# Performance work log

Hardware: AMD Instinct MI355X
Metric: run time of the kernel (lower is better)

The kernel has to match this reference:

```python
import jax, jax.numpy as jnp
import numpy as np

NUM_HEADS = 32
NUM_KV_HEADS = 8
HEAD_DIM = 128
SEQ = 2048
MAX_SLOTS = 4096
SCALE = float(1.0 / np.sqrt(HEAD_DIM))  # attn_scale
G = NUM_HEADS // NUM_KV_HEADS  # num_queries_per_kv


def setup_inputs() -> dict:
    key = jax.random.key(0)
    k1, k2, k3 = jax.random.split(key, 3)
    q = jax.random.normal(k1, (SEQ, NUM_HEADS, HEAD_DIM), dtype=jnp.float32)
    k = jax.random.normal(k2, (SEQ, NUM_KV_HEADS, HEAD_DIM), dtype=jnp.float32)
    v = jax.random.normal(k3, (SEQ, NUM_KV_HEADS, HEAD_DIM), dtype=jnp.float32)
    k_cache = jnp.zeros((MAX_SLOTS, NUM_KV_HEADS, HEAD_DIM), dtype=jnp.float32)
    v_cache = jnp.zeros((MAX_SLOTS, NUM_KV_HEADS, HEAD_DIM), dtype=jnp.float32)
    slot_mapping = jnp.arange(SEQ, dtype=jnp.int64)  # contiguous block_table slots
    return {"q": q, "k": k, "v": v, "k_cache": k_cache, "v_cache": v_cache,
            "slot_mapping": slot_mapping}


def reference(q, k, v, k_cache, v_cache, slot_mapping):
    # prefill: scatter-write new K/V into the paged cache (self.k_cache[slot_mapping] = k)
    kc = k_cache.at[slot_mapping].set(k)
    vc = v_cache.at[slot_mapping].set(v)
    # gather K/V back from the cache via slot mapping (paged gather pattern)
    k_attn = kc[slot_mapping]  # (S, Hkv, D) == k since slots are unique
    v_attn = vc[slot_mapping]
    # GQA: repeat_interleave kv heads to match query heads
    kr = jnp.repeat(k_attn, G, axis=1)  # (S, H, D)
    vr = jnp.repeat(v_attn, G, axis=1)
    # scores: (H, Sq, Sk), naive full materialization as in the original
    scores = jnp.einsum('qhd,khd->hqk', q, kr) * SCALE
    sq, sk = q.shape[0], k_attn.shape[0]
    mask = jnp.tril(jnp.ones((sq, sk), dtype=bool))  # causal (num_query_tokens > 1)
    scores = jnp.where(mask[None, :, :], scores, -jnp.inf)
    weights = jax.nn.softmax(scores, axis=-1)
    out = jnp.einsum('hqk,khd->qhd', weights, vr)  # (S, H, D)
    return out
```

## Files before the change

kernel.cpp:

```cpp
#include <hip/hip_runtime.h>
#include <hip/hip_bf16.h>

#define SEQ 2048
#define QSTR 4096
#define CSCALE 0.1275174364688796f

typedef __attribute__((ext_vector_type(8)))  short short8;
typedef __attribute__((ext_vector_type(4)))  float f32x4;
typedef __attribute__((ext_vector_type(16))) float f32x16;

union PF8 { unsigned u[4]; short8 s; };

__device__ __forceinline__ unsigned short f2bf(float f) {
    union { __hip_bfloat16 b; unsigned short u; } cv;
    cv.b = __float2bfloat16(f);
    return cv.u;
}
__device__ __forceinline__ float bf2f(unsigned short u) {
    unsigned v = ((unsigned)u) << 16;
    return __builtin_bit_cast(float, v);
}

__device__ __forceinline__ void gload16(const unsigned short* g, unsigned short* l) {
    __builtin_amdgcn_global_load_lds(
        (const __attribute__((address_space(1))) void*)g,
        (__attribute__((address_space(3))) void*)l, 16, 0, 0);
}

__global__ void prep_k(const float* __restrict__ Kg, unsigned short* __restrict__ Kb) {
    int gi = blockIdx.x * 256 + threadIdx.x;
    int kv = gi >> 8;
    int rem = gi & 255;
    int hk = rem >> 5;
    int d4 = rem & 31;
    f32x4 k4 = *(const f32x4*)(Kg + ((size_t)kv * 8 + hk) * 128 + 4 * d4);
    ushort4 u = make_ushort4(f2bf(k4[0]), f2bf(k4[1]), f2bf(k4[2]), f2bf(k4[3]));
    *(ushort4*)(Kb + ((size_t)hk * SEQ + kv) * 128 + 4 * d4) = u;
}

__global__ void prep_v(const float* __restrict__ Vg, unsigned short* __restrict__ Vtb) {
    const int hk  = blockIdx.x >> 5;
    const int kvb = blockIdx.x & 31;
    __shared__ unsigned short T[128][72];
    const int t = threadIdx.x;
    #pragma unroll
    for (int i = 0; i < 8; ++i) {
        int idx = t + 256 * i;
        int r = idx >> 5, d4 = idx & 31;
        f32x4 v = *(const f32x4*)(Vg + ((size_t)(kvb * 64 + r) * 8 + hk) * 128 + 4 * d4);
        T[4 * d4 + 0][r] = f2bf(v[0]);
        T[4 * d4 + 1][r] = f2bf(v[1]);
        T[4 * d4 + 2][r] = f2bf(v[2]);
        T[4 * d4 + 3][r] = f2bf(v[3]);
    }
    __syncthreads();
    #pragma unroll
    for (int i = 0; i < 8; ++i) {
        int idx = t + 256 * i;
        int d = idx >> 4, c4 = idx & 15;
        ushort4 u = *(ushort4*)&T[d][4 * c4];
        *(ushort4*)(Vtb + ((size_t)hk * 128 + d) * SEQ + kvb * 64 + 4 * c4) = u;
    }
}

__launch_bounds__(256, 2)
__global__ void attn_fwd(const float* __restrict__ Qg,
                         const unsigned short* __restrict__ Kb,
                         const unsigned short* __restrict__ Vtb,
                         float* __restrict__ Og) {
    const int bid = blockIdx.x;
    const int p   = bid >> 5;
    const int h   = bid & 31;
    const int hk  = h >> 2;
    const int qbB = 31 - p;
    const int qbA = p;
    const int nsB = 32 - p;

    const int tid  = threadIdx.x;
    const int w    = tid >> 6;
    const int b    = w & 1;
    const int hf   = w >> 1;
    const int lane = tid & 63;
    const int q5   = lane & 31;
    const int t5   = lane >> 5;

    __shared__ unsigned short Ks[2][64][128];
    __shared__ unsigned short Vp[2][64][128];
    __shared__ float mstat[2][4][32];
    __shared__ unsigned short Otb[32][136];

    short8 qf[8];
    auto LOADQ = [&](int qb) __attribute__((always_inline)) {
        const float* qp = Qg + (size_t)(qb * 64 + 32 * b + q5) * QSTR + h * 128 + 8 * t5;
        #pragma unroll
        for (int st = 0; st < 8; ++st) {
            f32x4 a = *(const f32x4*)(qp + 16 * st);
            f32x4 c = *(const f32x4*)(qp + 16 * st + 4);
            short8 f;
            f[0] = (short)f2bf(a[0] * CSCALE); f[1] = (short)f2bf(a[1] * CSCALE);
            f[2] = (short)f2bf(a[2] * CSCALE); f[3] = (short)f2bf(a[3] * CSCALE);
            f[4] = (short)f2bf(c[0] * CSCALE); f[5] = (short)f2bf(c[1] * CSCALE);
            f[6] = (short)f2bf(c[2] * CSCALE); f[7] = (short)f2bf(c[3] * CSCALE);
            qf[st] = f;
        }
    };

    auto ISSUE = [&](int kv0, int bb) __attribute__((always_inline)) {
        #pragma unroll
        for (int p4 = 0; p4 < 4; ++p4) {
            int row = 16 * w + 4 * p4 + (lane >> 4);
            const unsigned short* g = Kb +
                ((size_t)hk * SEQ + kv0 + row) * 128 + 8 * ((lane & 15) ^ (row & 15));
            gload16(g, &Ks[bb][16 * w + 4 * p4][0]);
        }
        #pragma unroll
        for (int p4 = 0; p4 < 4; ++p4) {
            int r  = 16 * w + 4 * p4 + (lane >> 4);
            int gg = lane & 15;
            int d  = 2 * r + (gg >> 3);
            int c  = (gg & 7) ^ (r & 7);
            const unsigned short* g = Vtb +
                ((size_t)hk * 128 + d) * SEQ + kv0 + 8 * c;
            gload16(g, &Vp[bb][16 * w + 4 * p4][0]);
        }
    };

    f32x16 oacc[4];
    float m, l;
    auto RESET = [&]() __attribute__((always_inline)) {
        #pragma unroll
        for (int dt = 0; dt < 4; ++dt)
            #pragma unroll
            for (int r = 0; r < 16; ++r) oacc[dt][r] = 0.f;
        m = -1e30f; l = 0.f;
    };

    auto EPI = [&](int qb) __attribute__((always_inline)) {
        if (t5 == 0) mstat[0][w][q5] = m;
        asm volatile("s_waitcnt lgkmcnt(0)" ::: "memory");
        __builtin_amdgcn_sched_barrier(0);
        __builtin_amdgcn_s_barrier();
        const float mo = mstat[0][w ^ 2][q5];
        const float M  = fmaxf(m, mo);
        const float sc = exp2f(m - M);
        #pragma unroll
        for (int dt = 0; dt < 4; ++dt)
            #pragma unroll
            for (int r = 0; r < 16; ++r) oacc[dt][r] *= sc;
        const float lp = l * sc;
        if (t5 == 0) mstat[1][w][q5] = lp;
        asm volatile("s_waitcnt lgkmcnt(0)" ::: "memory");
        __builtin_amdgcn_sched_barrier(0);
        __builtin_amdgcn_s_barrier();
        const float rl = 1.0f / (lp + mstat[1][w ^ 2][q5]);

        #pragma unroll 1
        for (int bb = 0; bb < 2; ++bb) {
            if (w == 2 + bb) {
                #pragma unroll
                for (int dt = 0; dt < 4; ++dt)
                    #pragma unroll
                    for (int ii = 0; ii < 4; ++ii) {
                        ushort4 u = make_ushort4(
                            f2bf(oacc[dt][4 * ii + 0]), f2bf(oacc[dt][4 * ii + 1]),
                            f2bf(oacc[dt][4 * ii + 2]), f2bf(oacc[dt][4 * ii + 3]));
                        *(ushort4*)&Otb[q5][32 * dt + 8 * ii + 4 * t5] = u;
                    }
            }
            asm volatile("s_waitcnt lgkmcnt(0)" ::: "memory");
            __builtin_amdgcn_sched_barrier(0);
            __builtin_amdgcn_s_barrier();
            if (w == bb) {
                #pragma unroll
                for (int dt = 0; dt < 4; ++dt)
                    #pragma unroll
                    for (int ii = 0; ii < 4; ++ii) {
                        ushort4 o1 = *(ushort4*)&Otb[q5][32 * dt + 8 * ii + 4 * t5];
                        ushort4 u = make_ushort4(
                            f2bf((oacc[dt][4 * ii + 0] + bf2f(o1.x)) * rl),
                            f2bf((oacc[dt][4 * ii + 1] + bf2f(o1.y)) * rl),
                            f2bf((oacc[dt][4 * ii + 2] + bf2f(o1.z)) * rl),
                            f2bf((oacc[dt][4 * ii + 3] + bf2f(o1.w)) * rl));
                        *(ushort4*)&Otb[q5][32 * dt + 8 * ii + 4 * t5] = u;
                    }
            }
            asm volatile("s_waitcnt lgkmcnt(0)" ::: "memory");
            __builtin_amdgcn_sched_barrier(0);
            __builtin_amdgcn_s_barrier();
            {
                const int r  = tid >> 3;
                const int c0 = 16 * (tid & 7);
                float* og = Og + (size_t)(qb * 64 + 32 * bb + r) * QSTR + h * 128 + c0;
                #pragma unroll
                for (int j = 0; j < 4; ++j) {
                    ushort4 u = *(ushort4*)&Otb[r][c0 + 4 * j];
                    f32x4 v;
                    v[0] = bf2f(u.x); v[1] = bf2f(u.y);
                    v[2] = bf2f(u.z); v[3] = bf2f(u.w);
                    *(f32x4*)(og + 4 * j) = v;
                }
            }
            asm volatile("s_waitcnt lgkmcnt(0)" ::: "memory");
            __builtin_amdgcn_sched_barrier(0);
            __builtin_amdgcn_s_barrier();
        }
    };

    LOADQ(qbB);
    #pragma unroll
    for (int st = 0; st < 8; ++st) asm volatile("" :: "v"(qf[st]));
    asm volatile("s_waitcnt vmcnt(0)" ::: "memory");
    RESET();

    ISSUE(0, 0);
    ISSUE(64, 1);

    for (int s = 0; s < 33; ++s) {
        if (s == nsB) {
            LOADQ(qbA);
            EPI(qbB);
            RESET();
        }
        const bool isB = (s < nsB);
        const int kv0  = isB ? 64 * s : 64 * (s - nsB);
        const int qb   = isB ? qbB : qbA;
        const int q0w  = qb * 64 + 32 * b;
        const int buf  = s & 1;

        if (s + 1 < 33) asm volatile("s_waitcnt vmcnt(8)" ::: "memory");
        else            asm volatile("s_waitcnt vmcnt(0)" ::: "memory");
        __builtin_amdgcn_s_barrier();

        const int kvh = kv0 + 32 * hf;
        if (kvh <= q0w + 31) {
            f32x16 sac;
            #pragma unroll
            for (int r = 0; r < 16; ++r) sac[r] = 0.f;
            __builtin_amdgcn_s_setprio(1);
            #pragma unroll
            for (int st = 0; st < 8; ++st) {
                short8 kf = *(const short8*)
                    &Ks[buf][32 * hf + q5][8 * ((2 * st + t5) ^ (q5 & 15))];
                sac = __builtin_amdgcn_mfma_f32_32x32x16_bf16(kf, qf[st], sac, 0, 0, 0);
            }
            __builtin_amdgcn_s_setprio(0);

            if (kvh + 31 > q0w) {
                const int qrow = q0w + q5;
                #pragma unroll
                for (int r = 0; r < 16; ++r) {
                    int kv = kvh + (r & 3) + 8 * (r >> 2) + 4 * t5;
                    if (kv > qrow) sac[r] = -1e30f;
                }
            }

            float m8[8], m4[4], m2[2];
            #pragma unroll
            for (int i = 0; i < 8; ++i) m8[i] = fmaxf(sac[i], sac[i + 8]);
            #pragma unroll
            for (int i = 0; i < 4; ++i) m4[i] = fmaxf(m8[i], m8[i + 4]);
            m2[0] = fmaxf(m4[0], m4[2]); m2[1] = fmaxf(m4[1], m4[3]);
            float mx = fmaxf(m2[0], m2[1]);
            mx = fmaxf(mx, __shfl_xor(mx, 32));

            const bool skip = __all(mx <= m + 11.0f);
            float fac = 1.0f;
            if (!skip) {
                float mn = fmaxf(m, mx);
                fac = exp2f(m - mn);
                m = mn;
            }

            #pragma unroll
            for (int r = 0; r < 16; ++r) sac[r] = exp2f(sac[r] - m);
            float s8[8], s4[4], s2[2];
            #pragma unroll
            for (int i = 0; i < 8; ++i) s8[i] = sac[i] + sac[i + 8];
            #pragma unroll
            for (int i = 0; i < 4; ++i) s4[i] = s8[i] + s8[i + 4];
            s2[0] = s4[0] + s4[2]; s2[1] = s4[1] + s4[3];
            float ps = s2[0] + s2[1];
            ps += __shfl_xor(ps, 32);
            if (!skip) {
                l = l * fac + ps;
                #pragma unroll
                for (int dt = 0; dt < 4; ++dt)
                    #pragma unroll
                    for (int r = 0; r < 16; ++r) oacc[dt][r] *= fac;
            } else {
                l += ps;
            }

            unsigned pkw[8];
            #pragma unroll
            for (int rp = 0; rp < 8; ++rp)
                pkw[rp] = (unsigned)f2bf(sac[2 * rp]) |
                          ((unsigned)f2bf(sac[2 * rp + 1]) << 16);

            unsigned xp[8];
            #pragma unroll
            for (int i = 0; i < 8; ++i)
                xp[i] = (unsigned)__shfl_xor((int)pkw[i], 32);

            PF8 pf[2];
            #pragma unroll
            for (int ks = 0; ks < 2; ++ks) {
                #pragma unroll
                for (int j = 0; j < 4; ++j) {
                    const int ib = (j & 1) + 4 * ks;
                    const unsigned own_lo = pkw[ib];
                    const unsigned own_hi = pkw[ib + 2];
                    const unsigned par_lo = xp[ib];
                    const unsigned par_hi = xp[ib + 2];
                    pf[ks].u[j] = (j < 2) ? (t5 ? par_hi : own_lo)
                                          : (t5 ? own_hi : par_lo);
                }
            }

            __builtin_amdgcn_s_setprio(1);
            #pragma unroll
            for (int dt = 0; dt < 4; ++dt) {
                #pragma unroll
                for (int ks = 0; ks < 2; ++ks) {
                    const int gg = 8 * (q5 & 1) +
                        ((4 * hf + 2 * ks + t5) ^ ((q5 >> 1) & 7));
                    short8 vf = *(const short8*)
                        &Vp[buf][16 * dt + (q5 >> 1)][8 * gg];
                    oacc[dt] = __builtin_amdgcn_mfma_f32_32x32x16_bf16(vf, pf[ks].s, oacc[dt], 0, 0, 0);
                }
            }
            __builtin_amdgcn_s_setprio(0);
        }

        asm volatile("" ::: "memory");
        __builtin_amdgcn_s_barrier();
        if (s + 2 < 33) {
            const int s2 = s + 2;
            ISSUE((s2 < nsB) ? 64 * s2 : 64 * (s2 - nsB), s & 1);
        }
    }

    EPI(qbA);
}

extern "C" void kernel_launch(void* const* d_in, const int* in_sizes, int n_in,
                              void* d_out, int out_size, void* d_ws, size_t ws_size,
                              hipStream_t stream) {
    const float* q = (const float*)d_in[0];
    const float* k = (const float*)d_in[1];
    const float* v = (const float*)d_in[2];
    float* out = (float*)d_out;
    unsigned short* Kb  = (unsigned short*)d_ws;
    unsigned short* Vtb = Kb + (size_t)8 * SEQ * 128;
    prep_k<<<dim3(2048), 256, 0, stream>>>(k, Kb);
    prep_v<<<dim3(256), 256, 0, stream>>>(v, Vtb);
    attn_fwd<<<dim3(512), 256, 0, stream>>>(q, Kb, Vtb, out);
}
```

Baseline: 90.90 us.

## Load K/V fragments directly into registers, drop LDS staging, use 32-row query tiles

Removes the shared-memory double-buffered K/V staging with async global-to-LDS loads. Each wave now reads its K and transposed-V MFMA operands straight from global memory into registers and prefetches the next tiles in software. Query tiles shrink to 32 rows, with 2-wave blocks of 128 threads and 1024 blocks, pairing tiles p and 63-p for causal balance. This drops LDS traffic and per-iteration barriers, but K/V reuse across waves now depends on the L2/L1 caches and register pressure rises.

```diff
diff --git a/kernel.cpp b/kernel.cpp
--- a/kernel.cpp
+++ b/kernel.cpp
@@ -19,12 +19,6 @@
 __device__ __forceinline__ float bf2f(unsigned short u) {
     unsigned v = ((unsigned)u) << 16;
     return __builtin_bit_cast(float, v);
-}
-
-__device__ __forceinline__ void gload16(const unsigned short* g, unsigned short* l) {
-    __builtin_amdgcn_global_load_lds(
-        (const __attribute__((address_space(1))) void*)g,
-        (__attribute__((address_space(3))) void*)l, 16, 0, 0);
 }
 
 __global__ void prep_k(const float* __restrict__ Kg, unsigned short* __restrict__ Kb) {
@@ -63,7 +57,7 @@
     }
 }
 
-__launch_bounds__(256, 2)
+__launch_bounds__(128, 2)
 __global__ void attn_fwd(const float* __restrict__ Qg,
                          const unsigned short* __restrict__ Kb,
                          const unsigned short* __restrict__ Vtb,
@@ -72,75 +66,179 @@
     const int p   = bid >> 5;
     const int h   = bid & 31;
     const int hk  = h >> 2;
-    const int qbB = 31 - p;
-    const int qbA = p;
-    const int nsB = 32 - p;
+    const int tb  = 63 - p;
+    const int ta  = p;
 
     const int tid  = threadIdx.x;
-    const int w    = tid >> 6;
-    const int b    = w & 1;
-    const int hf   = w >> 1;
+    const int wk   = tid >> 6;
     const int lane = tid & 63;
     const int q5   = lane & 31;
     const int t5   = lane >> 5;
 
-    __shared__ unsigned short Ks[2][64][128];
-    __shared__ unsigned short Vp[2][64][128];
-    __shared__ float mstat[2][4][32];
+    __shared__ float mstat[2][2][32];
     __shared__ unsigned short Otb[32][136];
 
-    short8 qf[8];
-    auto LOADQ = [&](int qb) __attribute__((always_inline)) {
-        const float* qp = Qg + (size_t)(qb * 64 + 32 * b + q5) * QSTR + h * 128 + 8 * t5;
-        #pragma unroll
-        for (int st = 0; st < 8; ++st) {
-            f32x4 a = *(const f32x4*)(qp + 16 * st);
-            f32x4 c = *(const f32x4*)(qp + 16 * st + 4);
-            short8 f;
-            f[0] = (short)f2bf(a[0] * CSCALE); f[1] = (short)f2bf(a[1] * CSCALE);
-            f[2] = (short)f2bf(a[2] * CSCALE); f[3] = (short)f2bf(a[3] * CSCALE);
-            f[4] = (short)f2bf(c[0] * CSCALE); f[5] = (short)f2bf(c[1] * CSCALE);
-            f[6] = (short)f2bf(c[2] * CSCALE); f[7] = (short)f2bf(c[3] * CSCALE);
-            qf[st] = f;
-        }
-    };
-
-    auto ISSUE = [&](int kv0, int bb) __attribute__((always_inline)) {
-        #pragma unroll
-        for (int p4 = 0; p4 < 4; ++p4) {
-            int row = 16 * w + 4 * p4 + (lane >> 4);
-            const unsigned short* g = Kb +
-                ((size_t)hk * SEQ + kv0 + row) * 128 + 8 * ((lane & 15) ^ (row & 15));
-            gload16(g, &Ks[bb][16 * w + 4 * p4][0]);
-        }
-        #pragma unroll
-        for (int p4 = 0; p4 < 4; ++p4) {
-            int r  = 16 * w + 4 * p4 + (lane >> 4);
-            int gg = lane & 15;
-            int d  = 2 * r + (gg >> 3);
-            int c  = (gg & 7) ^ (r & 7);
-            const unsigned short* g = Vtb +
-                ((size_t)hk * 128 + d) * SEQ + kv0 + 8 * c;
-            gload16(g, &Vp[bb][16 * w + 4 * p4][0]);
-        }
-    };
-
+    const unsigned short* Kh = Kb  + (size_t)hk * SEQ * 128;
+    const unsigned short* Vh = Vtb + (size_t)hk * 128 * SEQ;
+
+    short8 kA[8], kB[8], vR[8], qf[8];
     f32x16 oacc[4];
     float m, l;
-    auto RESET = [&]() __attribute__((always_inline)) {
+
+    auto LOADK = [&](short8 (&ks8)[8], int kv0) __attribute__((always_inline)) {
+        const unsigned short* kp = Kh + (size_t)(kv0 + q5) * 128 + 8 * t5;
+        #pragma unroll
+        for (int st = 0; st < 8; ++st)
+            ks8[st] = *(const short8*)(kp + 16 * st);
+    };
+    auto LOADV = [&](int kv0) __attribute__((always_inline)) {
+        #pragma unroll
+        for (int dt = 0; dt < 4; ++dt)
+            #pragma unroll
+            for (int ks = 0; ks < 2; ++ks)
+                vR[2 * dt + ks] = *(const short8*)
+                    (Vh + (size_t)(32 * dt + q5) * SEQ + kv0 + 16 * ks + 8 * t5);
+    };
+
+    auto STEP = [&](short8 (&kset)[8], int j, int q0, int qt, int nw)
+        __attribute__((always_inline)) {
+        const int kv0 = 32 * (2 * j + wk);
+
+        f32x16 sac;
+        #pragma unroll
+        for (int r = 0; r < 16; ++r) sac[r] = 0.f;
+        __builtin_amdgcn_s_setprio(1);
+        #pragma unroll
+        for (int st = 0; st < 8; ++st)
+            sac = __builtin_amdgcn_mfma_f32_32x32x16_bf16(kset[st], qf[st], sac, 0, 0, 0);
+        __builtin_amdgcn_s_setprio(0);
+
+        if (j + 2 < nw) LOADK(kset, 32 * (2 * j + 4 + wk));
+
+        if (kv0 + 31 > q0) {
+            const int qrow = q0 + q5;
+            #pragma unroll
+            for (int r = 0; r < 16; ++r) {
+                int kv = kv0 + (r & 3) + 8 * (r >> 2) + 4 * t5;
+                if (kv > qrow) sac[r] = -1e30f;
+            }
+        }
+
+        float m8[8], m4[4], m2[2];
+        #pragma unroll
+        for (int i = 0; i < 8; ++i) m8[i] = fmaxf(sac[i], sac[i + 8]);
+        #pragma unroll
+        for (int i = 0; i < 4; ++i) m4[i] = fmaxf(m8[i], m8[i + 4]);
+        m2[0] = fmaxf(m4[0], m4[2]); m2[1] = fmaxf(m4[1], m4[3]);
+        float mx = fmaxf(m2[0], m2[1]);
+        mx = fmaxf(mx, __shfl_xor(mx, 32));
+
+        const bool skip = __all(mx <= m + 11.0f);
+        float fac = 1.0f;
+        if (!skip) {
+            float mn = fmaxf(m, mx);
+            fac = exp2f(m - mn);
+            m = mn;
+        }
+
+        #pragma unroll
+        for (int r = 0; r < 16; ++r) sac[r] = exp2f(sac[r] - m);
+        float s8[8], s4[4], s2[2];
+        #pragma unroll
+        for (int i = 0; i < 8; ++i) s8[i] = sac[i] + sac[i + 8];
+        #pragma unroll
+        for (int i = 0; i < 4; ++i) s4[i] = s8[i] + s8[i + 4];
+        s2[0] = s4[0] + s4[2]; s2[1] = s4[1] + s4[3];
+        float ps = s2[0] + s2[1];
+        ps += __shfl_xor(ps, 32);
+        if (!skip) {
+            l = l * fac + ps;
+            #pragma unroll
+            for (int dt = 0; dt < 4; ++dt)
+                #pragma unroll
+                for (int r = 0; r < 16; ++r) oacc[dt][r] *= fac;
+        } else {
+            l += ps;
+        }
+
+        unsigned pkw[8];
+        #pragma unroll
+        for (int rp = 0; rp < 8; ++rp)
+            pkw[rp] = (unsigned)f2bf(sac[2 * rp]) |
+                      ((unsigned)f2bf(sac[2 * rp + 1]) << 16);
+
+        unsigned xp[8];
+        #pragma unroll
+        for (int i = 0; i < 8; ++i)
+            xp[i] = (unsigned)__shfl_xor((int)pkw[i], 32);
+
+        PF8 pf[2];
+        #pragma unroll
+        for (int ks = 0; ks < 2; ++ks) {
+            #pragma unroll
+            for (int j4 = 0; j4 < 4; ++j4) {
+                const int ib = (j4 & 1) + 4 * ks;
+                const unsigned own_lo = pkw[ib];
+                const unsigned own_hi = pkw[ib + 2];
+                const unsigned par_lo = xp[ib];
+                const unsigned par_hi = xp[ib + 2];
+                pf[ks].u[j4] = (j4 < 2) ? (t5 ? par_hi : own_lo)
+                                        : (t5 ? own_hi : par_lo);
+            }
+        }
+
+        __builtin_amdgcn_s_setprio(1);
+        #pragma unroll
+        for (int dt = 0; dt < 4; ++dt)
+            #pragma unroll
+            for (int ks = 0; ks < 2; ++ks)
+                oacc[dt] = __builtin_amdgcn_mfma_f32_32x32x16_bf16(
+                    vR[2 * dt + ks], pf[ks].s, oacc[dt], 0, 0, 0);
+        __builtin_amdgcn_s_setprio(0);
+
+        if (j + 1 < nw) LOADV(32 * (2 * j + 2 + wk));
+    };
+
+    #pragma unroll 1
+    for (int ph = 0; ph < 2; ++ph) {
+        const int qt = ph ? ta : tb;
+        const int q0 = 32 * qt;
+        const int nw = (qt + 2 - wk) >> 1;
+
+        {
+            const float* qp = Qg + (size_t)(q0 + q5) * QSTR + h * 128 + 8 * t5;
+            #pragma unroll
+            for (int st = 0; st < 8; ++st) {
+                f32x4 a = *(const f32x4*)(qp + 16 * st);
+                f32x4 c = *(const f32x4*)(qp + 16 * st + 4);
+                short8 f;
+                f[0] = (short)f2bf(a[0] * CSCALE); f[1] = (short)f2bf(a[1] * CSCALE);
+                f[2] = (short)f2bf(a[2] * CSCALE); f[3] = (short)f2bf(a[3] * CSCALE);
+                f[4] = (short)f2bf(c[0] * CSCALE); f[5] = (short)f2bf(c[1] * CSCALE);
+                f[6] = (short)f2bf(c[2] * CSCALE); f[7] = (short)f2bf(c[3] * CSCALE);
+                qf[st] = f;
+            }
+        }
         #pragma unroll
         for (int dt = 0; dt < 4; ++dt)
             #pragma unroll
             for (int r = 0; r < 16; ++r) oacc[dt][r] = 0.f;
         m = -1e30f; l = 0.f;
-    };
-
-    auto EPI = [&](int qb) __attribute__((always_inline)) {
-        if (t5 == 0) mstat[0][w][q5] = m;
-        asm volatile("s_waitcnt lgkmcnt(0)" ::: "memory");
-        __builtin_amdgcn_sched_barrier(0);
-        __builtin_amdgcn_s_barrier();
-        const float mo = mstat[0][w ^ 2][q5];
+
+        if (nw > 0) {
+            LOADK(kA, 32 * wk);
+            LOADV(32 * wk);
+            if (nw > 1) LOADK(kB, 32 * (2 + wk));
+            #pragma unroll 1
+            for (int j = 0; j < nw; j += 2) {
+                STEP(kA, j, q0, qt, nw);
+                if (j + 1 < nw) STEP(kB, j + 1, q0, qt, nw);
+            }
+        }
+
+        if (t5 == 0) mstat[0][wk][q5] = m;
+        __syncthreads();
+        const float mo = mstat[0][wk ^ 1][q5];
         const float M  = fmaxf(m, mo);
         const float sc = exp2f(m - M);
         #pragma unroll
@@ -148,199 +246,52 @@
             #pragma unroll
             for (int r = 0; r < 16; ++r) oacc[dt][r] *= sc;
         const float lp = l * sc;
-        if (t5 == 0) mstat[1][w][q5] = lp;
-        asm volatile("s_waitcnt lgkmcnt(0)" ::: "memory");
-        __builtin_amdgcn_sched_barrier(0);
-        __builtin_amdgcn_s_barrier();
-        const float rl = 1.0f / (lp + mstat[1][w ^ 2][q5]);
-
-        #pragma unroll 1
-        for (int bb = 0; bb < 2; ++bb) {
-            if (w == 2 + bb) {
+        if (t5 == 0) mstat[1][wk][q5] = lp;
+        __syncthreads();
+        const float rl = 1.0f / (lp + mstat[1][wk ^ 1][q5]);
+
+        if (wk == 1) {
+            #pragma unroll
+            for (int dt = 0; dt < 4; ++dt)
                 #pragma unroll
-                for (int dt = 0; dt < 4; ++dt)
-                    #pragma unroll
-                    for (int ii = 0; ii < 4; ++ii) {
-                        ushort4 u = make_ushort4(
-                            f2bf(oacc[dt][4 * ii + 0]), f2bf(oacc[dt][4 * ii + 1]),
-                            f2bf(oacc[dt][4 * ii + 2]), f2bf(oacc[dt][4 * ii + 3]));
-                        *(ushort4*)&Otb[q5][32 * dt + 8 * ii + 4 * t5] = u;
-                    }
-            }
-            asm volatile("s_waitcnt lgkmcnt(0)" ::: "memory");
-            __builtin_amdgcn_sched_barrier(0);
-            __builtin_amdgcn_s_barrier();
-            if (w == bb) {
+                for (int ii = 0; ii < 4; ++ii) {
+                    ushort4 u = make_ushort4(
+                        f2bf(oacc[dt][4 * ii + 0]), f2bf(oacc[dt][4 * ii + 1]),
+                        f2bf(oacc[dt][4 * ii + 2]), f2bf(oacc[dt][4 * ii + 3]));
+                    *(ushort4*)&Otb[q5][32 * dt + 8 * ii + 4 * t5] = u;
+                }
+        }
+        __syncthreads();
+        if (wk == 0) {
+            #pragma unroll
+            for (int dt = 0; dt < 4; ++dt)
                 #pragma unroll
-                for (int dt = 0; dt < 4; ++dt)
-                    #pragma unroll
-                    for (int ii = 0; ii < 4; ++ii) {
-                        ushort4 o1 = *(ushort4*)&Otb[q5][32 * dt + 8 * ii + 4 * t5];
-                        ushort4 u = make_ushort4(
-                            f2bf((oacc[dt][4 * ii + 0] + bf2f(o1.x)) * rl),
-                            f2bf((oacc[dt][4 * ii + 1] + bf2f(o1.y)) * rl),
-                            f2bf((oacc[dt][4 * ii + 2] + bf2f(o1.z)) * rl),
-                            f2bf((oacc[dt][4 * ii + 3] + bf2f(o1.w)) * rl));
-                        *(ushort4*)&Otb[q5][32 * dt + 8 * ii + 4 * t5] = u;
-                    }
-            }
-            asm volatile("s_waitcnt lgkmcnt(0)" ::: "memory");
-            __builtin_amdgcn_sched_barrier(0);
-            __builtin_amdgcn_s_barrier();
-            {
-                const int r  = tid >> 3;
-                const int c0 = 16 * (tid & 7);
-                float* og = Og + (size_t)(qb * 64 + 32 * bb + r) * QSTR + h * 128 + c0;
-                #pragma unroll
-                for (int j = 0; j < 4; ++j) {
-                    ushort4 u = *(ushort4*)&Otb[r][c0 + 4 * j];
-                    f32x4 v;
-                    v[0] = bf2f(u.x); v[1] = bf2f(u.y);
-                    v[2] = bf2f(u.z); v[3] = bf2f(u.w);
-                    *(f32x4*)(og + 4 * j) = v;
+                for (int ii = 0; ii < 4; ++ii) {
+                    ushort4 o1 = *(ushort4*)&Otb[q5][32 * dt + 8 * ii + 4 * t5];
+                    ushort4 u = make_ushort4(
+                        f2bf((oacc[dt][4 * ii + 0] + bf2f(o1.x)) * rl),
+                        f2bf((oacc[dt][4 * ii + 1] + bf2f(o1.y)) * rl),
+                        f2bf((oacc[dt][4 * ii + 2] + bf2f(o1.z)) * rl),
+                        f2bf((oacc[dt][4 * ii + 3] + bf2f(o1.w)) * rl));
+                    *(ushort4*)&Otb[q5][32 * dt + 8 * ii + 4 * t5] = u;
                 }
-            }
-            asm volatile("s_waitcnt lgkmcnt(0)" ::: "memory");
-            __builtin_amdgcn_sched_barrier(0);
-            __builtin_amdgcn_s_barrier();
-        }
-    };
-
-    LOADQ(qbB);
-    #pragma unroll
-    for (int st = 0; st < 8; ++st) asm volatile("" :: "v"(qf[st]));
-    asm volatile("s_waitcnt vmcnt(0)" ::: "memory");
-    RESET();
-
-    ISSUE(0, 0);
-    ISSUE(64, 1);
-
-    for (int s = 0; s < 33; ++s) {
-        if (s == nsB) {
-            LOADQ(qbA);
-            EPI(qbB);
-            RESET();
-        }
-        const bool isB = (s < nsB);
-        const int kv0  = isB ? 64 * s : 64 * (s - nsB);
-        const int qb   = isB ? qbB : qbA;
-        const int q0w  = qb * 64 + 32 * b;
-        const int buf  = s & 1;
-
-        if (s + 1 < 33) asm volatile("s_waitcnt vmcnt(8)" ::: "memory");
-        else            asm volatile("s_waitcnt vmcnt(0)" ::: "memory");
-        __builtin_amdgcn_s_barrier();
-
-        const int kvh = kv0 + 32 * hf;
-        if (kvh <= q0w + 31) {
-            f32x16 sac;
-            #pragma unroll
-            for (int r = 0; r < 16; ++r) sac[r] = 0.f;
-            __builtin_amdgcn_s_setprio(1);
-            #pragma unroll
-            for (int st = 0; st < 8; ++st) {
-                short8 kf = *(const short8*)
-                    &Ks[buf][32 * hf + q5][8 * ((2 * st + t5) ^ (q5 & 15))];
-                sac = __builtin_amdgcn_mfma_f32_32x32x16_bf16(kf, qf[st], sac, 0, 0, 0);
-            }
-            __builtin_amdgcn_s_setprio(0);
-
-            if (kvh + 31 > q0w) {
-                const int qrow = q0w + q5;
-                #pragma unroll
-                for (int r = 0; r < 16; ++r) {
-                    int kv = kvh + (r & 3) + 8 * (r >> 2) + 4 * t5;
-                    if (kv > qrow) sac[r] = -1e30f;
-                }
-            }
-
-            float m8[8], m4[4], m2[2];
-            #pragma unroll
-            for (int i = 0; i < 8; ++i) m8[i] = fmaxf(sac[i], sac[i + 8]);
-            #pragma unroll
-            for (int i = 0; i < 4; ++i) m4[i] = fmaxf(m8[i], m8[i + 4]);
-            m2[0] = fmaxf(m4[0], m4[2]); m2[1] = fmaxf(m4[1], m4[3]);
-            float mx = fmaxf(m2[0], m2[1]);
-            mx = fmaxf(mx, __shfl_xor(mx, 32));
-
-            const bool skip = __all(mx <= m + 11.0f);
-            float fac = 1.0f;
-            if (!skip) {
-                float mn = fmaxf(m, mx);
-                fac = exp2f(m - mn);
-                m = mn;
-            }
-
-            #pragma unroll
-            for (int r = 0; r < 16; ++r) sac[r] = exp2f(sac[r] - m);
-            float s8[8], s4[4], s2[2];
-            #pragma unroll
-            for (int i = 0; i < 8; ++i) s8[i] = sac[i] + sac[i + 8];
-            #pragma unroll
-            for (int i = 0; i < 4; ++i) s4[i] = s8[i] + s8[i + 4];
-            s2[0] = s4[0] + s4[2]; s2[1] = s4[1] + s4[3];
-            float ps = s2[0] + s2[1];
-            ps += __shfl_xor(ps, 32);
-            if (!skip) {
-                l = l * fac + ps;
-                #pragma unroll
-                for (int dt = 0; dt < 4; ++dt)
-                    #pragma unroll
-                    for (int r = 0; r < 16; ++r) oacc[dt][r] *= fac;
-            } else {
-                l += ps;
-            }
-
-            unsigned pkw[8];
-            #pragma unroll
-            for (int rp = 0; rp < 8; ++rp)
-                pkw[rp] = (unsigned)f2bf(sac[2 * rp]) |
-                          ((unsigned)f2bf(sac[2 * rp + 1]) << 16);
-
-            unsigned xp[8];
-            #pragma unroll
-            for (int i = 0; i < 8; ++i)
-                xp[i] = (unsigned)__shfl_xor((int)pkw[i], 32);
-
-            PF8 pf[2];
-            #pragma unroll
-            for (int ks = 0; ks < 2; ++ks) {
-                #pragma unroll
-                for (int j = 0; j < 4; ++j) {
-                    const int ib = (j & 1) + 4 * ks;
-                    const unsigned own_lo = pkw[ib];
-                    const unsigned own_hi = pkw[ib + 2];
-                    const unsigned par_lo = xp[ib];
-                    const unsigned par_hi = xp[ib + 2];
-                    pf[ks].u[j] = (j < 2) ? (t5 ? par_hi : own_lo)
-                                          : (t5 ? own_hi : par_lo);
-                }
-            }
-
-            __builtin_amdgcn_s_setprio(1);
-            #pragma unroll
-            for (int dt = 0; dt < 4; ++dt) {
-                #pragma unroll
-                for (int ks = 0; ks < 2; ++ks) {
-                    const int gg = 8 * (q5 & 1) +
-                        ((4 * hf + 2 * ks + t5) ^ ((q5 >> 1) & 7));
-                    short8 vf = *(const short8*)
-                        &Vp[buf][16 * dt + (q5 >> 1)][8 * gg];
-                    oacc[dt] = __builtin_amdgcn_mfma_f32_32x32x16_bf16(vf, pf[ks].s, oacc[dt], 0, 0, 0);
-                }
-            }
-            __builtin_amdgcn_s_setprio(0);
-        }
-
-        asm volatile("" ::: "memory");
-        __builtin_amdgcn_s_barrier();
-        if (s + 2 < 33) {
-            const int s2 = s + 2;
-            ISSUE((s2 < nsB) ? 64 * s2 : 64 * (s2 - nsB), s & 1);
-        }
+        }
+        __syncthreads();
+        {
+            #pragma unroll
+            for (int i = 0; i < 8; ++i) {
+                int ck = tid + 128 * i;
+                int r  = ck >> 5;
+                int c4 = (ck & 31) * 4;
+                ushort4 u = *(ushort4*)&Otb[r][c4];
+                f32x4 v;
+                v[0] = bf2f(u.x); v[1] = bf2f(u.y);
+                v[2] = bf2f(u.z); v[3] = bf2f(u.w);
+                *(f32x4*)(Og + (size_t)(q0 + r) * QSTR + h * 128 + c4) = v;
+            }
+        }
+        __syncthreads();
     }
-
-    EPI(qbA);
 }
 
 extern "C" void kernel_launch(void* const* d_in, const int* in_sizes, int n_in,
@@ -354,5 +305,5 @@
     unsigned short* Vtb = Kb + (size_t)8 * SEQ * 128;
     prep_k<<<dim3(2048), 256, 0, stream>>>(k, Kb);
     prep_v<<<dim3(256), 256, 0, stream>>>(v, Vtb);
-    attn_fwd<<<dim3(512), 256, 0, stream>>>(q, Kb, Vtb, out);
-}
+    attn_fwd<<<dim3(1024), 128, 0, stream>>>(q, Kb, Vtb, out);
+}
```

Result: slower. 155.8 us (+71.4%).

## Prefetch next tile's K/V MFMA fragments from LDS into registers

Applied to the files above, without the earlier changes.

Each iteration's K and V MFMA operands are now read from shared memory into register arrays at the end of the previous iteration, right after a single barrier. That barrier also publishes the next tile, and the global-to-LDS load for the tile after it is then issued. This cuts the loop from two barriers to one and moves the LDS fragment reads off the critical path ahead of the QK and PV MFMAs. In exchange it adds about 64 VGPRs of live fragment state, which risks lower occupancy or spills. It also waits for all outstanding vector memory before each barrier instead of keeping one tile in flight.

```diff
diff --git a/kernel.cpp b/kernel.cpp
--- a/kernel.cpp
+++ b/kernel.cpp
@@ -89,7 +89,8 @@
     __shared__ float mstat[2][4][32];
     __shared__ unsigned short Otb[32][136];
 
-    short8 qf[8];
+    short8 qf[8], kreg[8], vreg[8];
+
     auto LOADQ = [&](int qb) __attribute__((always_inline)) {
         const float* qp = Qg + (size_t)(qb * 64 + 32 * b + q5) * QSTR + h * 128 + 8 * t5;
         #pragma unroll
@@ -123,6 +124,22 @@
                 ((size_t)hk * 128 + d) * SEQ + kv0 + 8 * c;
             gload16(g, &Vp[bb][16 * w + 4 * p4][0]);
         }
+    };
+
+    auto RFRAGS = [&](int bb) __attribute__((always_inline)) {
+        #pragma unroll
+        for (int st = 0; st < 8; ++st)
+            kreg[st] = *(const short8*)
+                &Ks[bb][32 * hf + q5][8 * ((2 * st + t5) ^ (q5 & 15))];
+        #pragma unroll
+        for (int dt = 0; dt < 4; ++dt)
+            #pragma unroll
+            for (int ks = 0; ks < 2; ++ks) {
+                const int gg = 8 * (q5 & 1) +
+                    ((4 * hf + 2 * ks + t5) ^ ((q5 >> 1) & 7));
+                vreg[2 * dt + ks] = *(const short8*)
+                    &Vp[bb][16 * dt + (q5 >> 1)][8 * gg];
+            }
     };
 
     f32x16 oacc[4];
@@ -207,13 +224,14 @@
     };
 
     LOADQ(qbB);
-    #pragma unroll
-    for (int st = 0; st < 8; ++st) asm volatile("" :: "v"(qf[st]));
-    asm volatile("s_waitcnt vmcnt(0)" ::: "memory");
     RESET();
 
     ISSUE(0, 0);
     ISSUE(64, 1);
+    asm volatile("s_waitcnt vmcnt(0) lgkmcnt(0)" ::: "memory");
+    __builtin_amdgcn_s_barrier();
+    asm volatile("" ::: "memory");
+    RFRAGS(0);
 
     for (int s = 0; s < 33; ++s) {
         if (s == nsB) {
@@ -225,24 +243,16 @@
         const int kv0  = isB ? 64 * s : 64 * (s - nsB);
         const int qb   = isB ? qbB : qbA;
         const int q0w  = qb * 64 + 32 * b;
-        const int buf  = s & 1;
-
-        if (s + 1 < 33) asm volatile("s_waitcnt vmcnt(8)" ::: "memory");
-        else            asm volatile("s_waitcnt vmcnt(0)" ::: "memory");
-        __builtin_amdgcn_s_barrier();
-
-        const int kvh = kv0 + 32 * hf;
+        const int kvh  = kv0 + 32 * hf;
+
         if (kvh <= q0w + 31) {
             f32x16 sac;
             #pragma unroll
             for (int r = 0; r < 16; ++r) sac[r] = 0.f;
             __builtin_amdgcn_s_setprio(1);
             #pragma unroll
-            for (int st = 0; st < 8; ++st) {
-                short8 kf = *(const short8*)
-                    &Ks[buf][32 * hf + q5][8 * ((2 * st + t5) ^ (q5 & 15))];
-                sac = __builtin_amdgcn_mfma_f32_32x32x16_bf16(kf, qf[st], sac, 0, 0, 0);
-            }
+            for (int st = 0; st < 8; ++st)
+                sac = __builtin_amdgcn_mfma_f32_32x32x16_bf16(kreg[st], qf[st], sac, 0, 0, 0);
             __builtin_amdgcn_s_setprio(0);
 
             if (kvh + 31 > q0w) {
@@ -319,24 +329,23 @@
 
             __builtin_amdgcn_s_setprio(1);
             #pragma unroll
-            for (int dt = 0; dt < 4; ++dt) {
-                #pragma unroll
-                for (int ks = 0; ks < 2; ++ks) {
-                    const int gg = 8 * (q5 & 1) +
-                        ((4 * hf + 2 * ks + t5) ^ ((q5 >> 1) & 7));
-                    short8 vf = *(const short8*)
-                        &Vp[buf][16 * dt + (q5 >> 1)][8 * gg];
-                    oacc[dt] = __builtin_amdgcn_mfma_f32_32x32x16_bf16(vf, pf[ks].s, oacc[dt], 0, 0, 0);
-                }
-            }
+            for (int dt = 0; dt < 4; ++dt)
+                #pragma unroll
+                for (int ks = 0; ks < 2; ++ks)
+                    oacc[dt] = __builtin_amdgcn_mfma_f32_32x32x16_bf16(
+                        vreg[2 * dt + ks], pf[ks].s, oacc[dt], 0, 0, 0);
             __builtin_amdgcn_s_setprio(0);
         }
 
-        asm volatile("" ::: "memory");
-        __builtin_amdgcn_s_barrier();
-        if (s + 2 < 33) {
-            const int s2 = s + 2;
-            ISSUE((s2 < nsB) ? 64 * s2 : 64 * (s2 - nsB), s & 1);
+        if (s + 1 < 33) {
+            asm volatile("s_waitcnt vmcnt(0) lgkmcnt(0)" ::: "memory");
+            __builtin_amdgcn_s_barrier();
+            asm volatile("" ::: "memory");
+            RFRAGS((s + 1) & 1);
+            if (s + 2 < 33) {
+                const int s2 = s + 2;
+                ISSUE((s2 < nsB) ? 64 * s2 : 64 * (s2 - nsB), s & 1);
+            }
         }
     }
 
```

Result: slower. 195.8 us (+115.4%).

## Switch attention to 128-row query blocks with 8 waves per workgroup

Applied to the files above, without the earlier changes.

Replaces the paired short/long causal query-block scheme (two 64-row blocks per workgroup, run one after the other) with a single 128-row query block per workgroup, processed by 8 waves (4 query bands × 2 KV halves). Each K/V tile loaded to LDS is now reused across twice as many query rows, and the block order schedules long-running causal blocks first to even out load. K fragments are preloaded into registers before the MFMA chain. The cost is higher register pressure from 512-thread blocks and a longer epilogue that merges the two KV halves over four serialized output slices.

```diff
diff --git a/kernel.cpp b/kernel.cpp
--- a/kernel.cpp
+++ b/kernel.cpp
@@ -63,35 +63,38 @@
     }
 }
 
-__launch_bounds__(256, 2)
+__launch_bounds__(512, 4)
 __global__ void attn_fwd(const float* __restrict__ Qg,
                          const unsigned short* __restrict__ Kb,
                          const unsigned short* __restrict__ Vtb,
                          float* __restrict__ Og) {
-    const int bid = blockIdx.x;
-    const int p   = bid >> 5;
-    const int h   = bid & 31;
-    const int hk  = h >> 2;
-    const int qbB = 31 - p;
-    const int qbA = p;
-    const int nsB = 32 - p;
+    const int bid  = blockIdx.x;
+    const int half = bid >> 8;
+    const int idx  = bid & 255;
+    const int jj   = idx >> 4;
+    const int j    = half ? jj : 15 - jj;
+    const int h    = (idx & 15) | (half << 4);
+    const int hk   = h >> 2;
+    const int ns   = 2 * (j + 1);
 
     const int tid  = threadIdx.x;
     const int w    = tid >> 6;
-    const int b    = w & 1;
-    const int hf   = w >> 1;
+    const int band = w & 3;
+    const int hf   = w >> 2;
     const int lane = tid & 63;
     const int q5   = lane & 31;
     const int t5   = lane >> 5;
 
     __shared__ unsigned short Ks[2][64][128];
     __shared__ unsigned short Vp[2][64][128];
-    __shared__ float mstat[2][4][32];
+    __shared__ float mstat[2][8][32];
     __shared__ unsigned short Otb[32][136];
 
+    const int q0w = 128 * j + 32 * band;
+
     short8 qf[8];
-    auto LOADQ = [&](int qb) __attribute__((always_inline)) {
-        const float* qp = Qg + (size_t)(qb * 64 + 32 * b + q5) * QSTR + h * 128 + 8 * t5;
+    {
+        const float* qp = Qg + (size_t)(q0w + q5) * QSTR + h * 128 + 8 * t5;
         #pragma unroll
         for (int st = 0; st < 8; ++st) {
             f32x4 a = *(const f32x4*)(qp + 16 * st);
@@ -103,146 +106,62 @@
             f[6] = (short)f2bf(c[2] * CSCALE); f[7] = (short)f2bf(c[3] * CSCALE);
             qf[st] = f;
         }
-    };
+    }
+    #pragma unroll
+    for (int st = 0; st < 8; ++st) asm volatile("" :: "v"(qf[st]));
+    asm volatile("s_waitcnt vmcnt(0)" ::: "memory");
 
     auto ISSUE = [&](int kv0, int bb) __attribute__((always_inline)) {
         #pragma unroll
-        for (int p4 = 0; p4 < 4; ++p4) {
-            int row = 16 * w + 4 * p4 + (lane >> 4);
+        for (int p4 = 0; p4 < 2; ++p4) {
+            int row = 8 * w + 4 * p4 + (lane >> 4);
             const unsigned short* g = Kb +
                 ((size_t)hk * SEQ + kv0 + row) * 128 + 8 * ((lane & 15) ^ (row & 15));
-            gload16(g, &Ks[bb][16 * w + 4 * p4][0]);
-        }
-        #pragma unroll
-        for (int p4 = 0; p4 < 4; ++p4) {
-            int r  = 16 * w + 4 * p4 + (lane >> 4);
+            gload16(g, &Ks[bb][8 * w + 4 * p4][0]);
+        }
+        #pragma unroll
+        for (int p4 = 0; p4 < 2; ++p4) {
+            int r  = 8 * w + 4 * p4 + (lane >> 4);
             int gg = lane & 15;
             int d  = 2 * r + (gg >> 3);
             int c  = (gg & 7) ^ (r & 7);
             const unsigned short* g = Vtb +
                 ((size_t)hk * 128 + d) * SEQ + kv0 + 8 * c;
-            gload16(g, &Vp[bb][16 * w + 4 * p4][0]);
+            gload16(g, &Vp[bb][8 * w + 4 * p4][0]);
         }
     };
 
     f32x16 oacc[4];
-    float m, l;
-    auto RESET = [&]() __attribute__((always_inline)) {
-        #pragma unroll
-        for (int dt = 0; dt < 4; ++dt)
-            #pragma unroll
-            for (int r = 0; r < 16; ++r) oacc[dt][r] = 0.f;
-        m = -1e30f; l = 0.f;
-    };
-
-    auto EPI = [&](int qb) __attribute__((always_inline)) {
-        if (t5 == 0) mstat[0][w][q5] = m;
-        asm volatile("s_waitcnt lgkmcnt(0)" ::: "memory");
-        __builtin_amdgcn_sched_barrier(0);
-        __builtin_amdgcn_s_barrier();
-        const float mo = mstat[0][w ^ 2][q5];
-        const float M  = fmaxf(m, mo);
-        const float sc = exp2f(m - M);
-        #pragma unroll
-        for (int dt = 0; dt < 4; ++dt)
-            #pragma unroll
-            for (int r = 0; r < 16; ++r) oacc[dt][r] *= sc;
-        const float lp = l * sc;
-        if (t5 == 0) mstat[1][w][q5] = lp;
-        asm volatile("s_waitcnt lgkmcnt(0)" ::: "memory");
-        __builtin_amdgcn_sched_barrier(0);
-        __builtin_amdgcn_s_barrier();
-        const float rl = 1.0f / (lp + mstat[1][w ^ 2][q5]);
-
-        #pragma unroll 1
-        for (int bb = 0; bb < 2; ++bb) {
-            if (w == 2 + bb) {
-                #pragma unroll
-                for (int dt = 0; dt < 4; ++dt)
-                    #pragma unroll
-                    for (int ii = 0; ii < 4; ++ii) {
-                        ushort4 u = make_ushort4(
-                            f2bf(oacc[dt][4 * ii + 0]), f2bf(oacc[dt][4 * ii + 1]),
-                            f2bf(oacc[dt][4 * ii + 2]), f2bf(oacc[dt][4 * ii + 3]));
-                        *(ushort4*)&Otb[q5][32 * dt + 8 * ii + 4 * t5] = u;
-                    }
-            }
-            asm volatile("s_waitcnt lgkmcnt(0)" ::: "memory");
-            __builtin_amdgcn_sched_barrier(0);
-            __builtin_amdgcn_s_barrier();
-            if (w == bb) {
-                #pragma unroll
-                for (int dt = 0; dt < 4; ++dt)
-                    #pragma unroll
-                    for (int ii = 0; ii < 4; ++ii) {
-                        ushort4 o1 = *(ushort4*)&Otb[q5][32 * dt + 8 * ii + 4 * t5];
-                        ushort4 u = make_ushort4(
-                            f2bf((oacc[dt][4 * ii + 0] + bf2f(o1.x)) * rl),
-                            f2bf((oacc[dt][4 * ii + 1] + bf2f(o1.y)) * rl),
-                            f2bf((oacc[dt][4 * ii + 2] + bf2f(o1.z)) * rl),
-                            f2bf((oacc[dt][4 * ii + 3] + bf2f(o1.w)) * rl));
-                        *(ushort4*)&Otb[q5][32 * dt + 8 * ii + 4 * t5] = u;
-                    }
-            }
-            asm volatile("s_waitcnt lgkmcnt(0)" ::: "memory");
-            __builtin_amdgcn_sched_barrier(0);
-            __builtin_amdgcn_s_barrier();
-            {
-                const int r  = tid >> 3;
-                const int c0 = 16 * (tid & 7);
-                float* og = Og + (size_t)(qb * 64 + 32 * bb + r) * QSTR + h * 128 + c0;
-                #pragma unroll
-                for (int j = 0; j < 4; ++j) {
-                    ushort4 u = *(ushort4*)&Otb[r][c0 + 4 * j];
-                    f32x4 v;
-                    v[0] = bf2f(u.x); v[1] = bf2f(u.y);
-                    v[2] = bf2f(u.z); v[3] = bf2f(u.w);
-                    *(f32x4*)(og + 4 * j) = v;
-                }
-            }
-            asm volatile("s_waitcnt lgkmcnt(0)" ::: "memory");
-            __builtin_amdgcn_sched_barrier(0);
-            __builtin_amdgcn_s_barrier();
-        }
-    };
-
-    LOADQ(qbB);
-    #pragma unroll
-    for (int st = 0; st < 8; ++st) asm volatile("" :: "v"(qf[st]));
-    asm volatile("s_waitcnt vmcnt(0)" ::: "memory");
-    RESET();
+    #pragma unroll
+    for (int dt = 0; dt < 4; ++dt)
+        #pragma unroll
+        for (int r = 0; r < 16; ++r) oacc[dt][r] = 0.f;
+    float m = -1e30f, l = 0.f;
 
     ISSUE(0, 0);
-    ISSUE(64, 1);
-
-    for (int s = 0; s < 33; ++s) {
-        if (s == nsB) {
-            LOADQ(qbA);
-            EPI(qbB);
-            RESET();
-        }
-        const bool isB = (s < nsB);
-        const int kv0  = isB ? 64 * s : 64 * (s - nsB);
-        const int qb   = isB ? qbB : qbA;
-        const int q0w  = qb * 64 + 32 * b;
-        const int buf  = s & 1;
-
-        if (s + 1 < 33) asm volatile("s_waitcnt vmcnt(8)" ::: "memory");
+    if (ns > 1) ISSUE(64, 1);
+
+    for (int s = 0; s < ns; ++s) {
+        const int kv0 = 64 * s;
+        const int buf = s & 1;
+        if (s + 1 < ns) asm volatile("s_waitcnt vmcnt(4)" ::: "memory");
         else            asm volatile("s_waitcnt vmcnt(0)" ::: "memory");
         __builtin_amdgcn_s_barrier();
 
         const int kvh = kv0 + 32 * hf;
         if (kvh <= q0w + 31) {
+            short8 kreg[8];
+            #pragma unroll
+            for (int st = 0; st < 8; ++st)
+                kreg[st] = *(const short8*)
+                    &Ks[buf][32 * hf + q5][8 * ((2 * st + t5) ^ (q5 & 15))];
             f32x16 sac;
             #pragma unroll
             for (int r = 0; r < 16; ++r) sac[r] = 0.f;
             __builtin_amdgcn_s_setprio(1);
             #pragma unroll
-            for (int st = 0; st < 8; ++st) {
-                short8 kf = *(const short8*)
-                    &Ks[buf][32 * hf + q5][8 * ((2 * st + t5) ^ (q5 & 15))];
-                sac = __builtin_amdgcn_mfma_f32_32x32x16_bf16(kf, qf[st], sac, 0, 0, 0);
-            }
+            for (int st = 0; st < 8; ++st)
+                sac = __builtin_amdgcn_mfma_f32_32x32x16_bf16(kreg[st], qf[st], sac, 0, 0, 0);
             __builtin_amdgcn_s_setprio(0);
 
             if (kvh + 31 > q0w) {
@@ -306,14 +225,14 @@
             #pragma unroll
             for (int ks = 0; ks < 2; ++ks) {
                 #pragma unroll
-                for (int j = 0; j < 4; ++j) {
-                    const int ib = (j & 1) + 4 * ks;
+                for (int jq = 0; jq < 4; ++jq) {
+                    const int ib = (jq & 1) + 4 * ks;
                     const unsigned own_lo = pkw[ib];
                     const unsigned own_hi = pkw[ib + 2];
                     const unsigned par_lo = xp[ib];
                     const unsigned par_hi = xp[ib + 2];
-                    pf[ks].u[j] = (j < 2) ? (t5 ? par_hi : own_lo)
-                                          : (t5 ? own_hi : par_lo);
+                    pf[ks].u[jq] = (jq < 2) ? (t5 ? par_hi : own_lo)
+                                            : (t5 ? own_hi : par_lo);
                 }
             }
 
@@ -334,13 +253,78 @@
 
         asm volatile("" ::: "memory");
         __builtin_amdgcn_s_barrier();
-        if (s + 2 < 33) {
-            const int s2 = s + 2;
-            ISSUE((s2 < nsB) ? 64 * s2 : 64 * (s2 - nsB), s & 1);
-        }
-    }
-
-    EPI(qbA);
+        if (s + 2 < ns) ISSUE(64 * (s + 2), s & 1);
+    }
+
+    if (t5 == 0) mstat[0][w][q5] = m;
+    asm volatile("s_waitcnt lgkmcnt(0)" ::: "memory");
+    __builtin_amdgcn_sched_barrier(0);
+    __builtin_amdgcn_s_barrier();
+    const float mo = mstat[0][w ^ 4][q5];
+    const float M  = fmaxf(m, mo);
+    const float sc = exp2f(m - M);
+    #pragma unroll
+    for (int dt = 0; dt < 4; ++dt)
+        #pragma unroll
+        for (int r = 0; r < 16; ++r) oacc[dt][r] *= sc;
+    const float lp = l * sc;
+    if (t5 == 0) mstat[1][w][q5] = lp;
+    asm volatile("s_waitcnt lgkmcnt(0)" ::: "memory");
+    __builtin_amdgcn_sched_barrier(0);
+    __builtin_amdgcn_s_barrier();
+    const float rl = 1.0f / (lp + mstat[1][w ^ 4][q5]);
+
+    #pragma unroll 1
+    for (int tq = 0; tq < 4; ++tq) {
+        if (w == tq + 4) {
+            #pragma unroll
+            for (int dt = 0; dt < 4; ++dt)
+                #pragma unroll
+                for (int ii = 0; ii < 4; ++ii) {
+                    ushort4 u = make_ushort4(
+                        f2bf(oacc[dt][4 * ii + 0]), f2bf(oacc[dt][4 * ii + 1]),
+                        f2bf(oacc[dt][4 * ii + 2]), f2bf(oacc[dt][4 * ii + 3]));
+                    *(ushort4*)&Otb[q5][32 * dt + 8 * ii + 4 * t5] = u;
+                }
+        }
+        asm volatile("s_waitcnt lgkmcnt(0)" ::: "memory");
+        __builtin_amdgcn_sched_barrier(0);
+        __builtin_amdgcn_s_barrier();
+        if (w == tq) {
+            #pragma unroll
+            for (int dt = 0; dt < 4; ++dt)
+                #pragma unroll
+                for (int ii = 0; ii < 4; ++ii) {
+                    ushort4 o1 = *(ushort4*)&Otb[q5][32 * dt + 8 * ii + 4 * t5];
+                    ushort4 u = make_ushort4(
+                        f2bf((oacc[dt][4 * ii + 0] + bf2f(o1.x)) * rl),
+                        f2bf((oacc[dt][4 * ii + 1] + bf2f(o1.y)) * rl),
+                        f2bf((oacc[dt][4 * ii + 2] + bf2f(o1.z)) * rl),
+                        f2bf((oacc[dt][4 * ii + 3] + bf2f(o1.w)) * rl));
+                    *(ushort4*)&Otb[q5][32 * dt + 8 * ii + 4 * t5] = u;
+                }
+        }
+        asm volatile("s_waitcnt lgkmcnt(0)" ::: "memory");
+        __builtin_amdgcn_sched_barrier(0);
+        __builtin_amdgcn_s_barrier();
+        {
+            float* ob = Og + (size_t)(128 * j + 32 * tq) * QSTR + h * 128;
+            #pragma unroll
+            for (int i = 0; i < 2; ++i) {
+                int u  = tid + 512 * i;
+                int r  = u >> 5;
+                int c4 = (u & 31) * 4;
+                ushort4 ub = *(ushort4*)&Otb[r][c4];
+                f32x4 v;
+                v[0] = bf2f(ub.x); v[1] = bf2f(ub.y);
+                v[2] = bf2f(ub.z); v[3] = bf2f(ub.w);
+                *(f32x4*)(ob + (size_t)r * QSTR + c4) = v;
+            }
+        }
+        asm volatile("s_waitcnt lgkmcnt(0)" ::: "memory");
+        __builtin_amdgcn_sched_barrier(0);
+        __builtin_amdgcn_s_barrier();
+    }
 }
 
 extern "C" void kernel_launch(void* const* d_in, const int* in_sizes, int n_in,
@@ -354,5 +338,5 @@
     unsigned short* Vtb = Kb + (size_t)8 * SEQ * 128;
     prep_k<<<dim3(2048), 256, 0, stream>>>(k, Kb);
     prep_v<<<dim3(256), 256, 0, stream>>>(v, Vtb);
-    attn_fwd<<<dim3(512), 256, 0, stream>>>(q, Kb, Vtb, out);
-}
+    attn_fwd<<<dim3(512), 512, 0, stream>>>(q, Kb, Vtb, out);
+}
```

Result: slower. 291.0 us (+220.1%).
